# Kernel optimization log

Measured on AMD Instinct MI355X. Metric: run time of the kernel, lower is better.

Reference implementation:

```python
import jax, jax.numpy as jnp
import numpy as np

# NF4 (NormalFloat4) codebook from bitsandbytes
NF4 = jnp.array([
    -1.0, -0.6961928009986877, -0.5250730514526367, -0.39491748809814453,
    -0.28444138169288635, -0.18477343022823334, -0.09105003625154495, 0.0,
    0.07958029955625534, 0.16093020141124725, 0.24611230194568634,
    0.33791524171829224, 0.44070982933044434, 0.5626170039176941,
    0.7229568362236023, 1.0], dtype=jnp.float32)

BLOCK = 64          # bnb default quantization block size
RANK = 8
ALPHA = 16
SCALING = ALPHA / RANK


def setup_inputs() -> dict:
    key = jax.random.key(0)
    k = jax.random.split(key, 6)
    B, S, I, O = 4, 2048, 4096, 4096
    x = jax.random.normal(k[0], (B, S, I), dtype=jnp.float32)
    w_codes = jax.random.randint(k[1], (O, I), 0, 16, dtype=jnp.int32)
    absmax = jax.random.uniform(k[2], (O, I // BLOCK), dtype=jnp.float32)
    bias = jax.random.normal(k[3], (O,), dtype=jnp.float32)
    lora_A = jax.random.normal(k[4], (I, RANK), dtype=jnp.float32) / np.sqrt(I)
    lora_B = jax.random.normal(k[5], (RANK, O), dtype=jnp.float32)
    return {"x": x, "w_codes": w_codes, "absmax": absmax, "bias": bias,
            "lora_A": lora_A, "lora_B": lora_B}


def reference(x, w_codes, absmax, bias, lora_A, lora_B):
    O, I = w_codes.shape
    # NF4 dequantize: code lookup scaled by per-block absmax -> W [O, I]
    W = (NF4[w_codes].reshape(O, I // BLOCK, BLOCK) * absmax[:, :, None]).reshape(O, I)
    base = jnp.einsum('bsi,oi->bso', x, W) + bias
    # low-rank LoRA branch (dropout=0 -> identity)
    lora = ((x @ lora_A) @ lora_B) * SCALING
    return base + lora
```

## Files before the change

### kernel.cpp

```cpp
#include <hip/hip_runtime.h>
#include <hip/hip_bf16.h>
#include <stdint.h>


typedef __bf16 bf16x8 __attribute__((ext_vector_type(8)));
typedef float  f32x4  __attribute__((ext_vector_type(4)));
typedef unsigned short u16x8 __attribute__((ext_vector_type(8)));

__constant__ float NF4_TAB[16] = {
    -1.0f, -0.6961928009986877f, -0.5250730514526367f, -0.39491748809814453f,
    -0.28444138169288635f, -0.18477343022823334f, -0.09105003625154495f, 0.0f,
    0.07958029955625534f, 0.16093020141124725f, 0.24611230194568634f,
    0.33791524171829224f, 0.44070982933044434f, 0.5626170039176941f,
    0.7229568362236023f, 1.0f};

__device__ __forceinline__ unsigned short f2bf(float f) {
    unsigned int u = __float_as_uint(f);
    u += 0x7FFFu + ((u >> 16) & 1u);
    return (unsigned short)(u >> 16);
}

#define CVT_BLOCKS 4096
#define BLD_BLOCKS 2048

__global__ __launch_bounds__(256) void prep_kernel(
    const float* __restrict__ x, unsigned short* __restrict__ xb, int n8,
    const int* __restrict__ codes, const float* __restrict__ absmax,
    const float* __restrict__ lA, const float* __restrict__ lB,
    unsigned short* __restrict__ W, int O, int I, int nW8) {
    if ((int)blockIdx.x < CVT_BLOCKS) {
        const int base = blockIdx.x * 256 + threadIdx.x;
        const int stride = CVT_BLOCKS * 256;
#pragma unroll
        for (int k = 0; k < 4; ++k) {
            const int i = base + k * stride;
            if (i < n8) {
                const float4* p = (const float4*)x + (long)i * 2;
                float4 a = p[0], b = p[1];
                u16x8 o;
                o[0] = f2bf(a.x); o[1] = f2bf(a.y); o[2] = f2bf(a.z); o[3] = f2bf(a.w);
                o[4] = f2bf(b.x); o[5] = f2bf(b.y); o[6] = f2bf(b.z); o[7] = f2bf(b.w);
                *((u16x8*)xb + i) = o;
            }
        }
    } else {
        const int base = (blockIdx.x - CVT_BLOCKS) * 256 + threadIdx.x;
        const int stride = BLD_BLOCKS * 256;
        const int gpr = I >> 3;
#pragma unroll
        for (int k = 0; k < 4; ++k) {
            const int g8 = base + k * stride;
            if (g8 < nW8) {
                const int o  = g8 / gpr;
                const int i0 = (g8 - o * gpr) << 3;
                float bo[8];
#pragma unroll
                for (int r = 0; r < 8; ++r) bo[r] = lB[(long)r * O + o] * 2.0f;
                const long bse = (long)o * I + i0;
                const int4* cp = (const int4*)(codes + bse);
                int4 c0 = cp[0], c1 = cp[1];
                const float am = absmax[o * (I >> 6) + (i0 >> 6)];
                int cc[8] = {c0.x, c0.y, c0.z, c0.w, c1.x, c1.y, c1.z, c1.w};
                u16x8 ov;
#pragma unroll
                for (int j = 0; j < 8; ++j) {
                    const float4* ap = (const float4*)(lA + (long)(i0 + j) * 8);
                    float4 a0 = ap[0], a1 = ap[1];
                    float wv = NF4_TAB[cc[j] & 15] * am;
                    wv += a0.x * bo[0] + a0.y * bo[1] + a0.z * bo[2] + a0.w * bo[3]
                        + a1.x * bo[4] + a1.y * bo[5] + a1.z * bo[6] + a1.w * bo[7];
                    ov[j] = f2bf(wv);
                }
                *(u16x8*)(W + bse) = ov;
            }
        }
    }
}

#define BM 256
#define BN 256
#define BK 64

#define GLOAD16(g, s) __builtin_amdgcn_global_load_lds(                     \
    (const __attribute__((address_space(1))) void*)(g),                     \
    (__attribute__((address_space(3))) void*)(s), 16, 0, 0)

#define STAGE(ptr, ldsbase) do {                                            \
    GLOAD16((ptr), (char*)(ldsbase) + ldsW);                                \
    GLOAD16((ptr) + SK, (char*)(ldsbase) + 8192 + ldsW); } while (0)

#define BAR() do { asm volatile("" ::: "memory");                           \
    __builtin_amdgcn_s_barrier(); asm volatile("" ::: "memory"); } while (0)

#define MFMA_QUAD(H, KQ, BREG)                                              \
    _Pragma("unroll") for (int mi = 0; mi < 4; ++mi)                        \
    _Pragma("unroll") for (int ni = 0; ni < 2; ++ni) {                      \
        acc[H][KQ][mi][ni] = __builtin_amdgcn_mfma_f32_16x16x32_bf16(       \
            a[mi][0], BREG[ni][0], acc[H][KQ][mi][ni], 0, 0, 0);            \
        acc[H][KQ][mi][ni] = __builtin_amdgcn_mfma_f32_16x16x32_bf16(       \
            a[mi][1], BREG[ni][1], acc[H][KQ][mi][ni], 0, 0, 0); }

__global__ __launch_bounds__(512, 2) void gemm_kernel(
    const unsigned short* __restrict__ A,
    const unsigned short* __restrict__ Bm,
    const float* __restrict__ bias,
    float* __restrict__ out, int M, int N, int K, int gx, int gy) {
    __shared__ char lds[65536];

    int bx, by;
    {
        const int bid = blockIdx.x;
        if ((gx & 7) == 0 && (gy & 7) == 0 && ((gx >> 3) * (gy >> 3)) == 8) {
            const int xcd = bid & 7, loc = bid >> 3;
            const int cxs = gx >> 3;
            const int cr = xcd / cxs, cc = xcd - cr * cxs;
            by = cr * 8 + (loc >> 3);
            bx = cc * 8 + (loc & 7);
        } else if (((gx * gy) & 7) == 0) {
            const int q = (gx * gy) >> 3;
            const int id = (bid & 7) * q + (bid >> 3);
            bx = id % gx; by = id / gx;
        } else { bx = bid % gx; by = bid / gx; }
    }

    const int t = threadIdx.x;
    const int w = t >> 6, l = t & 63;
    const int wr = w >> 2, wc = w & 3;
    const long mB = (long)by * BM;
    const long nB = (long)bx * BN;
    const int NT = K / BK;

    const int sRow = w * 8 + (l >> 3);
    const int sCol = ((l & 7) ^ (l >> 3)) << 3;
    const int ldsW = w * 1024;
    const long SK = 64L * K;
    const long HK = 128L * K;
    const unsigned short* gA = A  + (mB + sRow) * K + sCol;
    const unsigned short* gB = Bm + (nB + sRow) * K + sCol;

    const unsigned short* pA0 = gA + BK;
    const unsigned short* pA1 = gA + HK + BK;
    const unsigned short* pB0 = gB + BK;
    const unsigned short* pB1 = gB + HK + BK;

    const int fr = l & 15;
    const int aoff0 = fr * 128 + ((((l >> 4)) ^ (l & 7)) << 4);
    const int aoff1 = fr * 128 + (((4 + (l >> 4)) ^ (l & 7)) << 4);

    f32x4 acc[2][2][4][2];
#pragma unroll
    for (int h = 0; h < 2; ++h)
#pragma unroll
        for (int k = 0; k < 2; ++k)
#pragma unroll
            for (int mi = 0; mi < 4; ++mi)
#pragma unroll
                for (int ni = 0; ni < 2; ++ni)
                    acc[h][k][mi][ni] = (f32x4){0.f, 0.f, 0.f, 0.f};

    STAGE(gA,      lds + 0);
    STAGE(gA + HK, lds + 16384);
    STAGE(gB,      lds + 32768);
    STAGE(gB + HK, lds + 49152);
    asm volatile("s_waitcnt vmcnt(0)" ::: "memory");
    BAR();

    bf16x8 a[4][2], b0[2][2], b1[2][2];
    const char* Ab = lds + wr * 8192;
    const char* Bb = lds + 32768 + wc * 4096;

    for (int g = 0; g < NT; ++g) {
        const bool st = (g + 1 < NT);

#pragma unroll
        for (int mi = 0; mi < 4; ++mi) {
            a[mi][0] = *(const bf16x8*)(Ab + mi * 2048 + aoff0);
            a[mi][1] = *(const bf16x8*)(Ab + mi * 2048 + aoff1);
        }
#pragma unroll
        for (int ni = 0; ni < 2; ++ni) {
            b0[ni][0] = *(const bf16x8*)(Bb + ni * 2048 + aoff0);
            b0[ni][1] = *(const bf16x8*)(Bb + ni * 2048 + aoff1);
        }
        asm volatile("s_waitcnt vmcnt(2)" ::: "memory");
        asm volatile("s_waitcnt lgkmcnt(0)" ::: "memory");
        BAR();
        __builtin_amdgcn_s_setprio(1);
        MFMA_QUAD(0, 0, b0);
        __builtin_amdgcn_s_setprio(0);

#pragma unroll
        for (int ni = 0; ni < 2; ++ni) {
            b1[ni][0] = *(const bf16x8*)(Bb + 16384 + ni * 2048 + aoff0);
            b1[ni][1] = *(const bf16x8*)(Bb + 16384 + ni * 2048 + aoff1);
        }
        if (st) {
            STAGE(pA0, lds + 0);
            STAGE(pB0, lds + 32768);
            asm volatile("s_waitcnt vmcnt(4)" ::: "memory");
        } else {
            asm volatile("s_waitcnt vmcnt(0)" ::: "memory");
        }
        asm volatile("s_waitcnt lgkmcnt(0)" ::: "memory");
        BAR();
        __builtin_amdgcn_s_setprio(1);
        MFMA_QUAD(0, 1, b1);
        __builtin_amdgcn_s_setprio(0);

#pragma unroll
        for (int mi = 0; mi < 4; ++mi) {
            a[mi][0] = *(const bf16x8*)(Ab + 16384 + mi * 2048 + aoff0);
            a[mi][1] = *(const bf16x8*)(Ab + 16384 + mi * 2048 + aoff1);
        }
        if (st) STAGE(pB1, lds + 49152);
        asm volatile("s_waitcnt lgkmcnt(0)" ::: "memory");
        BAR();
        __builtin_amdgcn_s_setprio(1);
        MFMA_QUAD(1, 0, b0);
        __builtin_amdgcn_s_setprio(0);

        if (st) {
            STAGE(pA1, lds + 16384);
            asm volatile("s_waitcnt vmcnt(4)" ::: "memory");
        } else {
            asm volatile("s_waitcnt vmcnt(0)" ::: "memory");
        }
        BAR();
        __builtin_amdgcn_s_setprio(1);
        MFMA_QUAD(1, 1, b1);
        __builtin_amdgcn_s_setprio(0);

        pA0 += BK; pA1 += BK; pB0 += BK; pB1 += BK;
    }

    const int r4 = (l >> 4) * 4;
#pragma unroll
    for (int kq = 0; kq < 2; ++kq) {
        float bs[2];
#pragma unroll
        for (int ni = 0; ni < 2; ++ni)
            bs[ni] = bias[nB + kq * 128 + wc * 32 + ni * 16 + fr];
#pragma unroll
        for (int h = 0; h < 2; ++h)
#pragma unroll
            for (int mi = 0; mi < 4; ++mi)
#pragma unroll
                for (int r = 0; r < 4; ++r) {
                    long row = mB + h * 128 + wr * 64 + mi * 16 + r4 + r;
                    float* op = out + row * N + nB + kq * 128 + wc * 32 + fr;
#pragma unroll
                    for (int ni = 0; ni < 2; ++ni)
                        op[ni * 16] = acc[h][kq][mi][ni][r] + bs[ni];
                }
    }
}

__global__ void naive_kernel(const float* __restrict__ x, const int* __restrict__ codes,
                             const float* __restrict__ absmax, const float* __restrict__ bias,
                             const float* __restrict__ lA, const float* __restrict__ lB,
                             float* __restrict__ out, int M, int I, int O) {
    long idx = (long)blockIdx.x * 256 + threadIdx.x;
    if (idx >= (long)M * O) return;
    int o = (int)(idx % O);
    long m = idx / O;
    const float* xr = x + m * I;
    const int* cr = codes + (long)o * I;
    const float* ar = absmax + (long)o * (I >> 6);
    float acc = 0.f;
    float la[8] = {0, 0, 0, 0, 0, 0, 0, 0};
    for (int i = 0; i < I; ++i) {
        float xv = xr[i];
        acc += xv * NF4_TAB[cr[i] & 15] * ar[i >> 6];
        const float* av = lA + (long)i * 8;
#pragma unroll
        for (int r = 0; r < 8; ++r) la[r] += xv * av[r];
    }
    float lv = 0.f;
#pragma unroll
    for (int r = 0; r < 8; ++r) lv += la[r] * lB[(long)r * O + o];
    out[idx] = acc + bias[o] + 2.0f * lv;
}

extern "C" void kernel_launch(void* const* d_in, const int* in_sizes, int n_in,
                              void* d_out, int out_size, void* d_ws, size_t ws_size,
                              hipStream_t stream) {
    const float* x      = (const float*)d_in[0];
    const int*   codes  = (const int*)d_in[1];
    const float* absmax = (const float*)d_in[2];
    const float* bias   = (const float*)d_in[3];
    const float* lA     = (const float*)d_in[4];
    const float* lB     = (const float*)d_in[5];
    float* out = (float*)d_out;

    const int I = in_sizes[4] / 8;
    const int O = in_sizes[3];
    const int M = in_sizes[0] / I;
    const int K = I;

    const size_t need = (size_t)M * K * 2 + (size_t)O * K * 2;
    if (ws_size < need || (M % BM) || (O % BN) || (K % 2048) || (K / BK) < 2) {
        long tot = (long)M * O;
        naive_kernel<<<(int)((tot + 255) / 256), 256, 0, stream>>>(
            x, codes, absmax, bias, lA, lB, out, M, I, O);
        return;
    }

    unsigned short* xb = (unsigned short*)d_ws;
    unsigned short* wb = xb + (size_t)M * K;

    const int n8  = (M * K) / 8;
    const int nW8 = (O * K) / 8;
    prep_kernel<<<CVT_BLOCKS + BLD_BLOCKS, 256, 0, stream>>>(
        x, xb, n8, codes, absmax, lA, lB, wb, O, K, nW8);
    const int gx = O / BN, gy = M / BM;
    gemm_kernel<<<gx * gy, 512, 0, stream>>>(xb, wb, bias, out, M, O, K, gx, gy);
}
```

Before: 348.4 us.

## Fuse prep and GEMM into one persistent cooperative kernel with grid sync

```diff
diff --git a/kernel.cpp b/kernel.cpp
--- a/kernel.cpp
+++ b/kernel.cpp
@@ -1,6 +1,9 @@
 #include <hip/hip_runtime.h>
 #include <hip/hip_bf16.h>
+#include <hip/hip_cooperative_groups.h>
 #include <stdint.h>
+
+namespace cg = cooperative_groups;
 
 
 typedef __bf16 bf16x8 __attribute__((ext_vector_type(8)));
@@ -18,63 +21,6 @@
     unsigned int u = __float_as_uint(f);
     u += 0x7FFFu + ((u >> 16) & 1u);
     return (unsigned short)(u >> 16);
-}
-
-#define CVT_BLOCKS 4096
-#define BLD_BLOCKS 2048
-
-__global__ __launch_bounds__(256) void prep_kernel(
-    const float* __restrict__ x, unsigned short* __restrict__ xb, int n8,
-    const int* __restrict__ codes, const float* __restrict__ absmax,
-    const float* __restrict__ lA, const float* __restrict__ lB,
-    unsigned short* __restrict__ W, int O, int I, int nW8) {
-    if ((int)blockIdx.x < CVT_BLOCKS) {
-        const int base = blockIdx.x * 256 + threadIdx.x;
-        const int stride = CVT_BLOCKS * 256;
-#pragma unroll
-        for (int k = 0; k < 4; ++k) {
-            const int i = base + k * stride;
-            if (i < n8) {
-                const float4* p = (const float4*)x + (long)i * 2;
-                float4 a = p[0], b = p[1];
-                u16x8 o;
-                o[0] = f2bf(a.x); o[1] = f2bf(a.y); o[2] = f2bf(a.z); o[3] = f2bf(a.w);
-                o[4] = f2bf(b.x); o[5] = f2bf(b.y); o[6] = f2bf(b.z); o[7] = f2bf(b.w);
-                *((u16x8*)xb + i) = o;
-            }
-        }
-    } else {
-        const int base = (blockIdx.x - CVT_BLOCKS) * 256 + threadIdx.x;
-        const int stride = BLD_BLOCKS * 256;
-        const int gpr = I >> 3;
-#pragma unroll
-        for (int k = 0; k < 4; ++k) {
-            const int g8 = base + k * stride;
-            if (g8 < nW8) {
-                const int o  = g8 / gpr;
-                const int i0 = (g8 - o * gpr) << 3;
-                float bo[8];
-#pragma unroll
-                for (int r = 0; r < 8; ++r) bo[r] = lB[(long)r * O + o] * 2.0f;
-                const long bse = (long)o * I + i0;
-                const int4* cp = (const int4*)(codes + bse);
-                int4 c0 = cp[0], c1 = cp[1];
-                const float am = absmax[o * (I >> 6) + (i0 >> 6)];
-                int cc[8] = {c0.x, c0.y, c0.z, c0.w, c1.x, c1.y, c1.z, c1.w};
-                u16x8 ov;
-#pragma unroll
-                for (int j = 0; j < 8; ++j) {
-                    const float4* ap = (const float4*)(lA + (long)(i0 + j) * 8);
-                    float4 a0 = ap[0], a1 = ap[1];
-                    float wv = NF4_TAB[cc[j] & 15] * am;
-                    wv += a0.x * bo[0] + a0.y * bo[1] + a0.z * bo[2] + a0.w * bo[3]
-                        + a1.x * bo[4] + a1.y * bo[5] + a1.z * bo[6] + a1.w * bo[7];
-                    ov[j] = f2bf(wv);
-                }
-                *(u16x8*)(W + bse) = ov;
-            }
-        }
-    }
 }
 
 #define BM 256
@@ -100,13 +46,252 @@
         acc[H][KQ][mi][ni] = __builtin_amdgcn_mfma_f32_16x16x32_bf16(       \
             a[mi][1], BREG[ni][1], acc[H][KQ][mi][ni], 0, 0, 0); }
 
-__global__ __launch_bounds__(512, 2) void gemm_kernel(
+__device__ __forceinline__ void cvt_group(const float* __restrict__ x,
+                                          unsigned short* __restrict__ xb, int i) {
+    const float4* p = (const float4*)x + (long)i * 2;
+    float4 a = p[0], b = p[1];
+    u16x8 o;
+    o[0] = f2bf(a.x); o[1] = f2bf(a.y); o[2] = f2bf(a.z); o[3] = f2bf(a.w);
+    o[4] = f2bf(b.x); o[5] = f2bf(b.y); o[6] = f2bf(b.z); o[7] = f2bf(b.w);
+    *((u16x8*)xb + i) = o;
+}
+
+__device__ __forceinline__ void build_group(
+    const int* __restrict__ codes, const float* __restrict__ absmax,
+    const float* __restrict__ lA, const float* __restrict__ lB,
+    unsigned short* __restrict__ W, int O, int I, int g8) {
+    const int gpr = I >> 3;
+    const int o  = g8 / gpr;
+    const int i0 = (g8 - o * gpr) << 3;
+    float bo[8];
+#pragma unroll
+    for (int r = 0; r < 8; ++r) bo[r] = lB[(long)r * O + o] * 2.0f;
+    const long bse = (long)o * I + i0;
+    const int4* cp = (const int4*)(codes + bse);
+    int4 c0 = cp[0], c1 = cp[1];
+    const float am = absmax[o * (I >> 6) + (i0 >> 6)];
+    int cc[8] = {c0.x, c0.y, c0.z, c0.w, c1.x, c1.y, c1.z, c1.w};
+    u16x8 ov;
+#pragma unroll
+    for (int j = 0; j < 8; ++j) {
+        const float4* ap = (const float4*)(lA + (long)(i0 + j) * 8);
+        float4 a0 = ap[0], a1 = ap[1];
+        float wv = NF4_TAB[cc[j] & 15] * am;
+        wv += a0.x * bo[0] + a0.y * bo[1] + a0.z * bo[2] + a0.w * bo[3]
+            + a1.x * bo[4] + a1.y * bo[5] + a1.z * bo[6] + a1.w * bo[7];
+        ov[j] = f2bf(wv);
+    }
+    *(u16x8*)(W + bse) = ov;
+}
+
+__device__ __forceinline__ void gemm_tile(
+    char* lds,
     const unsigned short* __restrict__ A,
     const unsigned short* __restrict__ Bm,
     const float* __restrict__ bias,
-    float* __restrict__ out, int M, int N, int K, int gx, int gy) {
+    float* __restrict__ out, int N, int K, int bx, int by) {
+
+    const int t = threadIdx.x;
+    const int w = t >> 6, l = t & 63;
+    const int wr = w >> 2, wc = w & 3;
+    const long mB = (long)by * BM;
+    const long nB = (long)bx * BN;
+    const int NT = K / BK;
+
+    const int sRow = w * 8 + (l >> 3);
+    const int sCol = ((l & 7) ^ (l >> 3)) << 3;
+    const int ldsW = w * 1024;
+    const long SK = 64L * K;
+    const long HK = 128L * K;
+    const unsigned short* gA = A  + (mB + sRow) * K + sCol;
+    const unsigned short* gB = Bm + (nB + sRow) * K + sCol;
+
+    const unsigned short* pA0 = gA + BK;
+    const unsigned short* pA1 = gA + HK + BK;
+    const unsigned short* pB0 = gB + BK;
+    const unsigned short* pB1 = gB + HK + BK;
+
+    const int fr = l & 15;
+    const int aoff0 = fr * 128 + ((((l >> 4)) ^ (l & 7)) << 4);
+    const int aoff1 = fr * 128 + (((4 + (l >> 4)) ^ (l & 7)) << 4);
+
+    f32x4 acc[2][2][4][2];
+#pragma unroll
+    for (int h = 0; h < 2; ++h)
+#pragma unroll
+        for (int k = 0; k < 2; ++k)
+#pragma unroll
+            for (int mi = 0; mi < 4; ++mi)
+#pragma unroll
+                for (int ni = 0; ni < 2; ++ni)
+                    acc[h][k][mi][ni] = (f32x4){0.f, 0.f, 0.f, 0.f};
+
+    STAGE(gA,      lds + 0);
+    STAGE(gA + HK, lds + 16384);
+    STAGE(gB,      lds + 32768);
+    STAGE(gB + HK, lds + 49152);
+    asm volatile("s_waitcnt vmcnt(0)" ::: "memory");
+    BAR();
+
+    bf16x8 a[4][2], b0[2][2], b1[2][2];
+    const char* Ab = lds + wr * 8192;
+    const char* Bb = lds + 32768 + wc * 4096;
+
+    for (int g = 0; g < NT; ++g) {
+        const bool st = (g + 1 < NT);
+
+#pragma unroll
+        for (int mi = 0; mi < 4; ++mi) {
+            a[mi][0] = *(const bf16x8*)(Ab + mi * 2048 + aoff0);
+            a[mi][1] = *(const bf16x8*)(Ab + mi * 2048 + aoff1);
+        }
+#pragma unroll
+        for (int ni = 0; ni < 2; ++ni) {
+            b0[ni][0] = *(const bf16x8*)(Bb + ni * 2048 + aoff0);
+            b0[ni][1] = *(const bf16x8*)(Bb + ni * 2048 + aoff1);
+        }
+        asm volatile("s_waitcnt vmcnt(2)" ::: "memory");
+        asm volatile("s_waitcnt lgkmcnt(0)" ::: "memory");
+        BAR();
+        __builtin_amdgcn_s_setprio(1);
+        MFMA_QUAD(0, 0, b0);
+        __builtin_amdgcn_s_setprio(0);
+
+#pragma unroll
+        for (int ni = 0; ni < 2; ++ni) {
+            b1[ni][0] = *(const bf16x8*)(Bb + 16384 + ni * 2048 + aoff0);
+            b1[ni][1] = *(const bf16x8*)(Bb + 16384 + ni * 2048 + aoff1);
+        }
+        if (st) {
+            STAGE(pA0, lds + 0);
+            STAGE(pB0, lds + 32768);
+            asm volatile("s_waitcnt vmcnt(4)" ::: "memory");
+        } else {
+            asm volatile("s_waitcnt vmcnt(0)" ::: "memory");
+        }
+        asm volatile("s_waitcnt lgkmcnt(0)" ::: "memory");
+        BAR();
+        __builtin_amdgcn_s_setprio(1);
+        MFMA_QUAD(0, 1, b1);
+        __builtin_amdgcn_s_setprio(0);
+
+#pragma unroll
+        for (int mi = 0; mi < 4; ++mi) {
+            a[mi][0] = *(const bf16x8*)(Ab + 16384 + mi * 2048 + aoff0);
+            a[mi][1] = *(const bf16x8*)(Ab + 16384 + mi * 2048 + aoff1);
+        }
+        if (st) STAGE(pB1, lds + 49152);
+        asm volatile("s_waitcnt lgkmcnt(0)" ::: "memory");
+        BAR();
+        __builtin_amdgcn_s_setprio(1);
+        MFMA_QUAD(1, 0, b0);
+        __builtin_amdgcn_s_setprio(0);
+
+        if (st) {
+            STAGE(pA1, lds + 16384);
+            asm volatile("s_waitcnt vmcnt(4)" ::: "memory");
+        } else {
+            asm volatile("s_waitcnt vmcnt(0)" ::: "memory");
+        }
+        BAR();
+        __builtin_amdgcn_s_setprio(1);
+        MFMA_QUAD(1, 1, b1);
+        __builtin_amdgcn_s_setprio(0);
+
+        pA0 += BK; pA1 += BK; pB0 += BK; pB1 += BK;
+    }
+
+    const int r4 = (l >> 4) * 4;
+#pragma unroll
+    for (int kq = 0; kq < 2; ++kq) {
+        float bs[2];
+#pragma unroll
+        for (int ni = 0; ni < 2; ++ni)
+            bs[ni] = bias[nB + kq * 128 + wc * 32 + ni * 16 + fr];
+#pragma unroll
+        for (int h = 0; h < 2; ++h)
+#pragma unroll
+            for (int mi = 0; mi < 4; ++mi)
+#pragma unroll
+                for (int r = 0; r < 4; ++r) {
+                    long row = mB + h * 128 + wr * 64 + mi * 16 + r4 + r;
+                    float* op = out + row * N + nB + kq * 128 + wc * 32 + fr;
+#pragma unroll
+                    for (int ni = 0; ni < 2; ++ni)
+                        op[ni * 16] = acc[h][kq][mi][ni][r] + bs[ni];
+                }
+    }
+}
+
+__global__ __launch_bounds__(512, 2) void fused_kernel(
+    const float* __restrict__ x, const int* __restrict__ codes,
+    const float* __restrict__ absmax, const float* __restrict__ bias,
+    const float* __restrict__ lA, const float* __restrict__ lB,
+    unsigned short* __restrict__ xb, unsigned short* __restrict__ wb,
+    float* __restrict__ out, int M, int N, int K, int n8, int nW8) {
     __shared__ char lds[65536];
 
+    const int tid = blockIdx.x * blockDim.x + threadIdx.x;
+    const int NTH = gridDim.x * blockDim.x;
+
+    for (int i0 = tid; i0 < n8; i0 += 4 * NTH) {
+#pragma unroll
+        for (int u = 0; u < 4; ++u) {
+            const int i = i0 + u * NTH;
+            if (i < n8) cvt_group(x, xb, i);
+        }
+    }
+    for (int g0 = tid; g0 < nW8; g0 += 4 * NTH) {
+#pragma unroll
+        for (int u = 0; u < 4; ++u) {
+            const int g8 = g0 + u * NTH;
+            if (g8 < nW8) build_group(codes, absmax, lA, lB, wb, N, K, g8);
+        }
+    }
+
+    cg::this_grid().sync();
+
+#pragma unroll 1
+    for (int tt = 0; tt < 2; ++tt) {
+        const int vt  = blockIdx.x + tt * gridDim.x;
+        const int xcd = vt & 7, loc = vt >> 3;
+        const int cr = xcd >> 1, cc = xcd & 1;
+        const int by = cr * 8 + (loc >> 3);
+        const int bx = cc * 8 + (loc & 7);
+        gemm_tile(lds, xb, wb, bias, out, N, K, bx, by);
+    }
+}
+
+__global__ __launch_bounds__(256) void prep_kernel(
+    const float* __restrict__ x, unsigned short* __restrict__ xb, int n8,
+    const int* __restrict__ codes, const float* __restrict__ absmax,
+    const float* __restrict__ lA, const float* __restrict__ lB,
+    unsigned short* __restrict__ W, int O, int I, int nW8) {
+    const int CVT = 4096;
+    if ((int)blockIdx.x < CVT) {
+        const int base = blockIdx.x * 256 + threadIdx.x;
+        const int stride = CVT * 256;
+#pragma unroll
+        for (int k = 0; k < 4; ++k) {
+            const int i = base + k * stride;
+            if (i < n8) cvt_group(x, xb, i);
+        }
+    } else {
+        const int base = (blockIdx.x - CVT) * 256 + threadIdx.x;
+        const int stride = 2048 * 256;
+#pragma unroll
+        for (int k = 0; k < 4; ++k) {
+            const int g8 = base + k * stride;
+            if (g8 < nW8) build_group(codes, absmax, lA, lB, W, O, I, g8);
+        }
+    }
+}
+
+__global__ __launch_bounds__(512, 2) void gemm_kernel(
+    const unsigned short* __restrict__ A, const unsigned short* __restrict__ Bm,
+    const float* __restrict__ bias, float* __restrict__ out,
+    int M, int N, int K, int gx, int gy) {
+    __shared__ char lds[65536];
     int bx, by;
     {
         const int bid = blockIdx.x;
@@ -122,137 +307,7 @@
             bx = id % gx; by = id / gx;
         } else { bx = bid % gx; by = bid / gx; }
     }
-
-    const int t = threadIdx.x;
-    const int w = t >> 6, l = t & 63;
-    const int wr = w >> 2, wc = w & 3;
-    const long mB = (long)by * BM;
-    const long nB = (long)bx * BN;
-    const int NT = K / BK;
-
-    const int sRow = w * 8 + (l >> 3);
-    const int sCol = ((l & 7) ^ (l >> 3)) << 3;
-    const int ldsW = w * 1024;
-    const long SK = 64L * K;
-    const long HK = 128L * K;
-    const unsigned short* gA = A  + (mB + sRow) * K + sCol;
-    const unsigned short* gB = Bm + (nB + sRow) * K + sCol;
-
-    const unsigned short* pA0 = gA + BK;
-    const unsigned short* pA1 = gA + HK + BK;
-    const unsigned short* pB0 = gB + BK;
-    const unsigned short* pB1 = gB + HK + BK;
-
-    const int fr = l & 15;
-    const int aoff0 = fr * 128 + ((((l >> 4)) ^ (l & 7)) << 4);
-    const int aoff1 = fr * 128 + (((4 + (l >> 4)) ^ (l & 7)) << 4);
-
-    f32x4 acc[2][2][4][2];
-#pragma unroll
-    for (int h = 0; h < 2; ++h)
-#pragma unroll
-        for (int k = 0; k < 2; ++k)
-#pragma unroll
-            for (int mi = 0; mi < 4; ++mi)
-#pragma unroll
-                for (int ni = 0; ni < 2; ++ni)
-                    acc[h][k][mi][ni] = (f32x4){0.f, 0.f, 0.f, 0.f};
-
-    STAGE(gA,      lds + 0);
-    STAGE(gA + HK, lds + 16384);
-    STAGE(gB,      lds + 32768);
-    STAGE(gB + HK, lds + 49152);
-    asm volatile("s_waitcnt vmcnt(0)" ::: "memory");
-    BAR();
-
-    bf16x8 a[4][2], b0[2][2], b1[2][2];
-    const char* Ab = lds + wr * 8192;
-    const char* Bb = lds + 32768 + wc * 4096;
-
-    for (int g = 0; g < NT; ++g) {
-        const bool st = (g + 1 < NT);
-
-#pragma unroll
-        for (int mi = 0; mi < 4; ++mi) {
-            a[mi][0] = *(const bf16x8*)(Ab + mi * 2048 + aoff0);
-            a[mi][1] = *(const bf16x8*)(Ab + mi * 2048 + aoff1);
-        }
-#pragma unroll
-        for (int ni = 0; ni < 2; ++ni) {
-            b0[ni][0] = *(const bf16x8*)(Bb + ni * 2048 + aoff0);
-            b0[ni][1] = *(const bf16x8*)(Bb + ni * 2048 + aoff1);
-        }
-        asm volatile("s_waitcnt vmcnt(2)" ::: "memory");
-        asm volatile("s_waitcnt lgkmcnt(0)" ::: "memory");
-        BAR();
-        __builtin_amdgcn_s_setprio(1);
-        MFMA_QUAD(0, 0, b0);
-        __builtin_amdgcn_s_setprio(0);
-
-#pragma unroll
-        for (int ni = 0; ni < 2; ++ni) {
-            b1[ni][0] = *(const bf16x8*)(Bb + 16384 + ni * 2048 + aoff0);
-            b1[ni][1] = *(const bf16x8*)(Bb + 16384 + ni * 2048 + aoff1);
-        }
-        if (st) {
-            STAGE(pA0, lds + 0);
-            STAGE(pB0, lds + 32768);
-            asm volatile("s_waitcnt vmcnt(4)" ::: "memory");
-        } else {
-            asm volatile("s_waitcnt vmcnt(0)" ::: "memory");
-        }
-        asm volatile("s_waitcnt lgkmcnt(0)" ::: "memory");
-        BAR();
-        __builtin_amdgcn_s_setprio(1);
-        MFMA_QUAD(0, 1, b1);
-        __builtin_amdgcn_s_setprio(0);
-
-#pragma unroll
-        for (int mi = 0; mi < 4; ++mi) {
-            a[mi][0] = *(const bf16x8*)(Ab + 16384 + mi * 2048 + aoff0);
-            a[mi][1] = *(const bf16x8*)(Ab + 16384 + mi * 2048 + aoff1);
-        }
-        if (st) STAGE(pB1, lds + 49152);
-        asm volatile("s_waitcnt lgkmcnt(0)" ::: "memory");
-        BAR();
-        __builtin_amdgcn_s_setprio(1);
-        MFMA_QUAD(1, 0, b0);
-        __builtin_amdgcn_s_setprio(0);
-
-        if (st) {
-            STAGE(pA1, lds + 16384);
-            asm volatile("s_waitcnt vmcnt(4)" ::: "memory");
-        } else {
-            asm volatile("s_waitcnt vmcnt(0)" ::: "memory");
-        }
-        BAR();
-        __builtin_amdgcn_s_setprio(1);
-        MFMA_QUAD(1, 1, b1);
-        __builtin_amdgcn_s_setprio(0);
-
-        pA0 += BK; pA1 += BK; pB0 += BK; pB1 += BK;
-    }
-
-    const int r4 = (l >> 4) * 4;
-#pragma unroll
-    for (int kq = 0; kq < 2; ++kq) {
-        float bs[2];
-#pragma unroll
-        for (int ni = 0; ni < 2; ++ni)
-            bs[ni] = bias[nB + kq * 128 + wc * 32 + ni * 16 + fr];
-#pragma unroll
-        for (int h = 0; h < 2; ++h)
-#pragma unroll
-            for (int mi = 0; mi < 4; ++mi)
-#pragma unroll
-                for (int r = 0; r < 4; ++r) {
-                    long row = mB + h * 128 + wr * 64 + mi * 16 + r4 + r;
-                    float* op = out + row * N + nB + kq * 128 + wc * 32 + fr;
-#pragma unroll
-                    for (int ni = 0; ni < 2; ++ni)
-                        op[ni * 16] = acc[h][kq][mi][ni][r] + bs[ni];
-                }
-    }
+    gemm_tile(lds, A, Bm, bias, out, N, K, bx, by);
 }
 
 __global__ void naive_kernel(const float* __restrict__ x, const int* __restrict__ codes,
@@ -298,7 +353,9 @@
     const int K = I;
 
     const size_t need = (size_t)M * K * 2 + (size_t)O * K * 2;
-    if (ws_size < need || (M % BM) || (O % BN) || (K % 2048) || (K / BK) < 2) {
+    const bool shapes_ok = !(ws_size < need || (M % BM) || (O % BN) ||
+                             (K % 2048) || (K / BK) < 2);
+    if (!shapes_ok) {
         long tot = (long)M * O;
         naive_kernel<<<(int)((tot + 255) / 256), 256, 0, stream>>>(
             x, codes, absmax, bias, lA, lB, out, M, I, O);
@@ -307,11 +364,22 @@
 
     unsigned short* xb = (unsigned short*)d_ws;
     unsigned short* wb = xb + (size_t)M * K;
-
-    const int n8  = (M * K) / 8;
-    const int nW8 = (O * K) / 8;
-    prep_kernel<<<CVT_BLOCKS + BLD_BLOCKS, 256, 0, stream>>>(
-        x, xb, n8, codes, absmax, lA, lB, wb, O, K, nW8);
     const int gx = O / BN, gy = M / BM;
+    int n8  = (M * K) / 8;
+    int nW8 = (O * K) / 8;
+    int Mi = M, Ni = O, Ki = K;
+
+    if (gx == 16 && gy == 32) {
+        void* args[] = {(void*)&x, (void*)&codes, (void*)&absmax, (void*)&bias,
+                        (void*)&lA, (void*)&lB, (void*)&xb, (void*)&wb,
+                        (void*)&out, (void*)&Mi, (void*)&Ni, (void*)&Ki,
+                        (void*)&n8, (void*)&nW8};
+        hipLaunchCooperativeKernel((void*)fused_kernel, dim3(256), dim3(512),
+                                   args, 0, stream);
+        return;
+    }
+
+    prep_kernel<<<4096 + 2048, 256, 0, stream>>>(x, xb, n8, codes, absmax,
+                                                 lA, lB, wb, O, K, nW8);
     gemm_kernel<<<gx * gy, 512, 0, stream>>>(xb, wb, bias, out, M, O, K, gx, gy);
 }
```

Measured after the change: 395.2 us. 1.13x slower.
